# Optimization experiments

Measured on AMD Instinct MI355X. Metric: run time of the kernel, lower is better.

Reference implementation:

```python
import jax, jax.numpy as jnp
import numpy as np

T, B, S = 128, 128, 128
H, E, V, L = 1024, 512, 32000, 2


def setup_inputs() -> dict:
    key = jax.random.key(0)
    ks = jax.random.split(key, 16)
    s = 0.02
    inp = {
        "inputs": jax.random.randint(ks[0], (T, B), 0, V),
        "h0": jax.random.normal(ks[1], (L, B, H), jnp.float32) * 0.1,
        "c0": jax.random.normal(ks[2], (L, B, H), jnp.float32) * 0.1,
        "contexts": jax.random.normal(ks[3], (B, S, H), jnp.float32),
        "emb": jax.random.normal(ks[4], (V, E), jnp.float32) * s,
        "W_ih0": jax.random.normal(ks[5], (4 * H, E), jnp.float32) * s,
        "W_hh0": jax.random.normal(ks[6], (4 * H, H), jnp.float32) * s,
        "b_ih0": jnp.zeros((4 * H,), jnp.float32),
        "b_hh0": jnp.zeros((4 * H,), jnp.float32),
        "W_ih1": jax.random.normal(ks[7], (4 * H, H), jnp.float32) * s,
        "W_hh1": jax.random.normal(ks[8], (4 * H, H), jnp.float32) * s,
        "b_ih1": jnp.zeros((4 * H,), jnp.float32),
        "b_hh1": jnp.zeros((4 * H,), jnp.float32),
        "att_in_W": jax.random.normal(ks[9], (H, H), jnp.float32) * s,
        "att_in_b": jnp.zeros((H,), jnp.float32),
        "att_out_W": jax.random.normal(ks[10], (H, 2 * H), jnp.float32) * s,
        "att_out_b": jnp.zeros((H,), jnp.float32),
    }
    return inp


def _lstm_cell(x, h, c, Wih, Whh, bih, bhh):
    # torch.nn.LSTMCell: gates in (i, f, g, o) order
    gates = x @ Wih.T + bih + h @ Whh.T + bhh  # [B, 4H]
    i, f, g, o = jnp.split(gates, 4, axis=-1)
    c2 = jax.nn.sigmoid(f) * c + jax.nn.sigmoid(i) * jnp.tanh(g)
    h2 = jax.nn.sigmoid(o) * jnp.tanh(c2)
    return h2, c2


def reference(inputs, h0, c0, contexts, emb,
              W_ih0, W_hh0, b_ih0, b_hh0,
              W_ih1, W_hh1, b_ih1, b_hh1,
              att_in_W, att_in_b, att_out_W, att_out_b):
    layer_params = [(W_ih0, W_hh0, b_ih0, b_hh0), (W_ih1, W_hh1, b_ih1, b_hh1)]
    embs = emb[inputs]  # [T, B, E]

    def step(carry, x_t):
        h, c = carry  # each [L, B, H]
        x = x_t
        hs, cs = [], []
        for l, (Wih, Whh, bih, bhh) in enumerate(layer_params):
            h_l, c_l = _lstm_cell(x, h[l], c[l], Wih, Whh, bih, bhh)
            x = h_l  # dropout=0.0 / eval mode -> identity
            hs.append(h_l)
            cs.append(c_l)
        # global (Luong general) attention
        gamma = x @ att_in_W.T + att_in_b                     # [B, H]
        scores = jnp.einsum('bsh,bh->bs', contexts, gamma)    # [B, S]
        w = jax.nn.softmax(scores, axis=-1)
        c_t = jnp.einsum('bs,bsh->bh', w, contexts)           # [B, H]
        out = jnp.tanh(jnp.concatenate([c_t, x], axis=-1) @ att_out_W.T + att_out_b)
        return (jnp.stack(hs), jnp.stack(cs)), (out, w)

    (hT, cT), (outputs, attns) = jax.lax.scan(step, (h0, c0), embs)
    return outputs, hT, cT
```

## Files before the change

kernel.cpp:

```cpp
#include <hip/hip_runtime.h>

#define TT 128
#define BB 128
#define SS 128
#define HH 1024
#define EE 512
#define BH (BB*HH)

typedef unsigned short u16;
typedef __attribute__((ext_vector_type(8))) short s8v;
typedef __attribute__((ext_vector_type(4))) float f32x4;

__device__ __forceinline__ float b2f(u16 u) {
    union { unsigned int i; float f; } v; v.i = ((unsigned int)u) << 16; return v.f;
}
__device__ __forceinline__ u16 f2b(float f) {
    union { float f; unsigned int i; } v; v.f = f;
    unsigned int x = v.i;
    x = x + 0x7fffu + ((x >> 16) & 1u);
    return (u16)(x >> 16);
}
__device__ __forceinline__ float sigm(float x) {
    float t = __expf(-fabsf(x));
    float p = 1.0f / (1.0f + t);
    return x >= 0.0f ? p : 1.0f - p;
}
__device__ __forceinline__ float tanh_(float x) {
    float t = __expf(-2.0f * fabsf(x));
    float r = (1.0f - t) / (1.0f + t);
    return x >= 0.0f ? r : -r;
}

#define MFMA(a, b, c) __builtin_amdgcn_mfma_f32_16x16x32_bf16((a), (b), (c), 0, 0, 0)

__global__ __launch_bounds__(256)
void cvt_k(const float* __restrict__ s, u16* __restrict__ d, int n)
{
    const int i = (blockIdx.x * 256 + threadIdx.x) * 4;
    if (i < n) {
        const float4 v = *(const float4*)(s + i);
        ushort4 o;
        o.x = f2b(v.x); o.y = f2b(v.y); o.z = f2b(v.z); o.w = f2b(v.w);
        *(ushort4*)(d + i) = o;
    }
}

__global__ __launch_bounds__(128)
void gather_k(const int* __restrict__ toks, const float* __restrict__ emb,
              u16* __restrict__ X)
{
    const int row = blockIdx.x;
    const int tok = toks[row];
    const int c = threadIdx.x * 4;
    const float4 v = *(const float4*)(emb + (size_t)tok * EE + c);
    ushort4 o;
    o.x = f2b(v.x); o.y = f2b(v.y); o.z = f2b(v.z); o.w = f2b(v.w);
    *(ushort4*)(X + (size_t)row * EE + c) = o;
}

__global__ __launch_bounds__(256)
void init_k(const float* __restrict__ h0in,
            u16* __restrict__ h0ring, u16* __restrict__ h1init,
            int* __restrict__ barcnt)
{
    const int i = blockIdx.x * 256 + threadIdx.x;
    const u16 hb = f2b(h0in[i]);
    if (i < BH) h0ring[i] = hb;
    else        h1init[i - BH] = hb;
    if (i == 0) *barcnt = 0;
}

__global__ __launch_bounds__(512, 1)
void scan_k(const float* __restrict__ Wih0, const float* __restrict__ Whh0,
            const float* __restrict__ Wih1, const float* __restrict__ Whh1,
            const float* __restrict__ bih0, const float* __restrict__ bhh0,
            const float* __restrict__ bih1, const float* __restrict__ bhh1,
            const float* __restrict__ c0in,
            const u16* __restrict__ Xb,
            u16* __restrict__ h0ring,
            const u16* __restrict__ h1init,
            u16* __restrict__ H1all,
            float* __restrict__ outT,
            int* __restrict__ barcnt)
{
    extern __shared__ u16 lds[];
    u16* W0x = lds;
    u16* W0h = W0x + 16*4*16*8;
    u16* W1x = W0h + 32*4*16*8;
    u16* W1h = W1x + 32*4*16*8;
    float* gst = (float*)(W1h + 32*4*16*8);

    const int tid  = threadIdx.x;
    const int bk   = blockIdx.x;
    const int j0   = (((bk & 7) << 5) | (bk >> 3)) * 4;
    const int lane = tid & 63;
    const int w    = tid >> 6;
    const int l15  = lane & 15, quad = lane >> 4;

    auto loadW = [&](const float* src, int K, u16* dst) {
        const int ntup = (K / 32) * 4 * 16;
        for (int idx = tid; idx < ntup; idx += 512) {
            const int n = idx & 15, q = (idx >> 4) & 3, kc = idx >> 6;
            const int col = ((n >> 2) * HH) + j0 + (n & 3);
            const float* sp = src + (size_t)col * K + kc * 32 + q * 8;
            const float4 v0 = *(const float4*)(sp);
            const float4 v1 = *(const float4*)(sp + 4);
            u16* dp = dst + (size_t)idx * 8;
            dp[0] = f2b(v0.x); dp[1] = f2b(v0.y); dp[2] = f2b(v0.z); dp[3] = f2b(v0.w);
            dp[4] = f2b(v1.x); dp[5] = f2b(v1.y); dp[6] = f2b(v1.z); dp[7] = f2b(v1.w);
        }
    };
    loadW(Wih0, EE, W0x);
    loadW(Whh0, HH, W0h);
    loadW(Wih1, HH, W1x);
    loadW(Whh1, HH, W1h);

    const int prow = tid >> 2;
    const int pjj  = tid & 3;
    const int pj   = j0 + pjj;
    const int pw   = prow >> 4, pr16 = prow & 15;

    float c0 = c0in[(size_t)0 * BH + (size_t)prow * HH + pj];
    float c1 = c0in[(size_t)1 * BH + (size_t)prow * HH + pj];
    float b0[4], b1[4];
    #pragma unroll
    for (int g = 0; g < 4; ++g) {
        b0[g] = bih0[g * HH + pj] + bhh0[g * HH + pj];
        b1[g] = bih1[g * HH + pj] + bhh1[g * HH + pj];
    }

    __syncthreads();

    const int arow = w * 16 + l15;

    for (int p = 0; p <= TT; ++p) {
        f32x4 acc0 = (f32x4)0.0f, acc1 = (f32x4)0.0f;

        if (p < TT) {
            const u16* ap = Xb + ((size_t)p * BB + arow) * EE + quad * 8;
            #pragma unroll 8
            for (int kc = 0; kc < 16; ++kc) {
                s8v a = *(const s8v*)(ap + kc * 32);
                s8v b = *(const s8v*)(W0x + ((size_t)(kc * 4 + quad) * 16 + l15) * 8);
                acc0 = MFMA(a, b, acc0);
            }
        }

        if (p > 0) {
            if (tid == 0) {
                const int target = 256 * p;
                while (__hip_atomic_load(barcnt, __ATOMIC_RELAXED,
                                         __HIP_MEMORY_SCOPE_AGENT) < target) {
                    __builtin_amdgcn_s_sleep(2);
                }
            }
            __syncthreads();
            asm volatile("" ::: "memory");
        }

        const u16* h0p = h0ring + (size_t)p * BH;
        {
            const u16* ap = h0p + (size_t)arow * HH + quad * 8;
            if (p == 0) {
                #pragma unroll 8
                for (int kc = 0; kc < 32; ++kc) {
                    s8v a = *(const s8v*)(ap + kc * 32);
                    s8v b = *(const s8v*)(W0h + ((size_t)(kc * 4 + quad) * 16 + l15) * 8);
                    acc0 = MFMA(a, b, acc0);
                }
            } else if (p == TT) {
                #pragma unroll 8
                for (int kc = 0; kc < 32; ++kc) {
                    s8v a = *(const s8v*)(ap + kc * 32);
                    s8v b = *(const s8v*)(W1x + ((size_t)(kc * 4 + quad) * 16 + l15) * 8);
                    acc1 = MFMA(a, b, acc1);
                }
            } else {
                #pragma unroll 8
                for (int kc = 0; kc < 32; ++kc) {
                    s8v a = *(const s8v*)(ap + kc * 32);
                    s8v b0v = *(const s8v*)(W0h + ((size_t)(kc * 4 + quad) * 16 + l15) * 8);
                    s8v b1v = *(const s8v*)(W1x + ((size_t)(kc * 4 + quad) * 16 + l15) * 8);
                    acc0 = MFMA(a, b0v, acc0);
                    acc1 = MFMA(a, b1v, acc1);
                }
            }
        }
        if (p > 0) {
            const u16* h1p = (p == 1) ? h1init : (H1all + (size_t)(p - 2) * BH);
            const u16* ap = h1p + (size_t)arow * HH + quad * 8;
            #pragma unroll 8
            for (int kc = 0; kc < 32; ++kc) {
                s8v a = *(const s8v*)(ap + kc * 32);
                s8v b = *(const s8v*)(W1h + ((size_t)(kc * 4 + quad) * 16 + l15) * 8);
                acc1 = MFMA(a, b, acc1);
            }
        }

        if (p < TT) {
            #pragma unroll
            for (int r = 0; r < 4; ++r)
                gst[w * 320 + (quad * 4 + r) * 20 + l15] = acc0[r];
            __syncthreads();
            const float* gr = gst + pw * 320 + pr16 * 20;
            const float gi = gr[0 + pjj]  + b0[0];
            const float gf = gr[4 + pjj]  + b0[1];
            const float gg = gr[8 + pjj]  + b0[2];
            const float go = gr[12 + pjj] + b0[3];
            c0 = sigm(gf) * c0 + sigm(gi) * tanh_(gg);
            const float h = sigm(go) * tanh_(c0);
            h0ring[(size_t)(p + 1) * BH + (size_t)prow * HH + pj] = f2b(h);
            if (p == TT - 1) {
                outT[(size_t)0 * BH + (size_t)prow * HH + pj] = h;
                outT[(size_t)2 * BH + (size_t)prow * HH + pj] = c0;
            }
            __syncthreads();
        }
        if (p > 0) {
            #pragma unroll
            for (int r = 0; r < 4; ++r)
                gst[w * 320 + (quad * 4 + r) * 20 + l15] = acc1[r];
            __syncthreads();
            const float* gr = gst + pw * 320 + pr16 * 20;
            const float gi = gr[0 + pjj]  + b1[0];
            const float gf = gr[4 + pjj]  + b1[1];
            const float gg = gr[8 + pjj]  + b1[2];
            const float go = gr[12 + pjj] + b1[3];
            c1 = sigm(gf) * c1 + sigm(gi) * tanh_(gg);
            const float h = sigm(go) * tanh_(c1);
            H1all[(size_t)(p - 1) * BH + (size_t)prow * HH + pj] = f2b(h);
            if (p == TT) {
                outT[(size_t)1 * BH + (size_t)prow * HH + pj] = h;
                outT[(size_t)3 * BH + (size_t)prow * HH + pj] = c1;
            }
            __syncthreads();
        }

        if (p < TT && tid == 0) {
            __hip_atomic_fetch_add(barcnt, 1, __ATOMIC_RELEASE,
                                   __HIP_MEMORY_SCOPE_AGENT);
        }
    }
}

__global__ __launch_bounds__(256)
void gemm_bt_k(const u16* __restrict__ A1, int K1,
               const u16* __restrict__ A2, int K2,
               const u16* __restrict__ W, int ldw,
               const float* __restrict__ bias,
               u16* __restrict__ Cb, float* __restrict__ Cf,
               int N, int act)
{
    const int lane = threadIdx.x & 63;
    const int wave = threadIdx.x >> 6;
    const int l15 = lane & 15, quad = lane >> 4;
    const int n0 = blockIdx.x * 64;
    const int mrow = blockIdx.y * 64 + wave * 16;
    const int arow = mrow + l15;

    f32x4 acc[4];
    #pragma unroll
    for (int nt = 0; nt < 4; ++nt) acc[nt] = (f32x4)0.0f;

    const u16* wr0 = W + (size_t)(n0 + 0 * 16 + l15) * ldw + quad * 8;
    const u16* wr1 = W + (size_t)(n0 + 1 * 16 + l15) * ldw + quad * 8;
    const u16* wr2 = W + (size_t)(n0 + 2 * 16 + l15) * ldw + quad * 8;
    const u16* wr3 = W + (size_t)(n0 + 3 * 16 + l15) * ldw + quad * 8;

    {
        const u16* ap = A1 + (size_t)arow * K1 + quad * 8;
        #pragma unroll 4
        for (int kk = 0; kk < K1; kk += 32) {
            s8v a = *(const s8v*)(ap + kk);
            acc[0] = MFMA(a, *(const s8v*)(wr0 + kk), acc[0]);
            acc[1] = MFMA(a, *(const s8v*)(wr1 + kk), acc[1]);
            acc[2] = MFMA(a, *(const s8v*)(wr2 + kk), acc[2]);
            acc[3] = MFMA(a, *(const s8v*)(wr3 + kk), acc[3]);
        }
    }
    if (A2 != nullptr) {
        const u16* ap = A2 + (size_t)arow * K2 + quad * 8;
        #pragma unroll 4
        for (int kk = 0; kk < K2; kk += 32) {
            s8v a = *(const s8v*)(ap + kk);
            acc[0] = MFMA(a, *(const s8v*)(wr0 + K1 + kk), acc[0]);
            acc[1] = MFMA(a, *(const s8v*)(wr1 + K1 + kk), acc[1]);
            acc[2] = MFMA(a, *(const s8v*)(wr2 + K1 + kk), acc[2]);
            acc[3] = MFMA(a, *(const s8v*)(wr3 + K1 + kk), acc[3]);
        }
    }
    #pragma unroll
    for (int nt = 0; nt < 4; ++nt) {
        const int col = n0 + nt * 16 + l15;
        const float bv = bias[col];
        #pragma unroll
        for (int r = 0; r < 4; ++r) {
            const int row = mrow + quad * 4 + r;
            float v = acc[nt][r] + bv;
            if (act) v = tanh_(v);
            if (Cf) Cf[(size_t)row * N + col] = v;
            else    Cb[(size_t)row * N + col] = f2b(v);
        }
    }
}

__global__ __launch_bounds__(256)
void attn_k(const u16* __restrict__ gamma, const float* __restrict__ ctx,
            u16* __restrict__ ctall)
{
    const int b = blockIdx.x;
    const int t0 = blockIdx.y * 16;
    const int tid = threadIdx.x;
    const int lane = tid & 63, wave = tid >> 6;
    const int l15 = lane & 15, quad = lane >> 4;

    __shared__ float sw[16 * SS];

    {
        f32x4 acc0 = (f32x4)0.0f, acc1 = (f32x4)0.0f;
        const u16*   ap  = gamma + ((size_t)(t0 + l15) * BB + b) * HH + quad * 8;
        const float* bp0 = ctx + ((size_t)b * SS + (wave * 32 + l15)) * HH + quad * 8;
        const float* bp1 = ctx + ((size_t)b * SS + (wave * 32 + 16 + l15)) * HH + quad * 8;
        for (int kk = 0; kk < HH; kk += 32) {
            s8v a = *(const s8v*)(ap + kk);
            float4 u0 = *(const float4*)(bp0 + kk);
            float4 u1 = *(const float4*)(bp0 + kk + 4);
            s8v bv;
            bv[0] = (short)f2b(u0.x); bv[1] = (short)f2b(u0.y);
            bv[2] = (short)f2b(u0.z); bv[3] = (short)f2b(u0.w);
            bv[4] = (short)f2b(u1.x); bv[5] = (short)f2b(u1.y);
            bv[6] = (short)f2b(u1.z); bv[7] = (short)f2b(u1.w);
            acc0 = MFMA(a, bv, acc0);
            float4 w0 = *(const float4*)(bp1 + kk);
            float4 w1 = *(const float4*)(bp1 + kk + 4);
            s8v cv;
            cv[0] = (short)f2b(w0.x); cv[1] = (short)f2b(w0.y);
            cv[2] = (short)f2b(w0.z); cv[3] = (short)f2b(w0.w);
            cv[4] = (short)f2b(w1.x); cv[5] = (short)f2b(w1.y);
            cv[6] = (short)f2b(w1.z); cv[7] = (short)f2b(w1.w);
            acc1 = MFMA(a, cv, acc1);
        }
        #pragma unroll
        for (int r = 0; r < 4; ++r) {
            const int trow = quad * 4 + r;
            sw[trow * SS + wave * 32 + l15] = acc0[r];
            sw[trow * SS + wave * 32 + 16 + l15] = acc1[r];
        }
    }
    __syncthreads();

    {
        const int row = tid >> 4, c0 = tid & 15;
        float e[8];
        float m = -1e30f;
        #pragma unroll
        for (int k = 0; k < 8; ++k) { e[k] = sw[row * SS + c0 + k * 16]; m = fmaxf(m, e[k]); }
        #pragma unroll
        for (int off = 8; off >= 1; off >>= 1) m = fmaxf(m, __shfl_xor(m, off));
        float s = 0.0f;
        #pragma unroll
        for (int k = 0; k < 8; ++k) { e[k] = __expf(e[k] - m); s += e[k]; }
        #pragma unroll
        for (int off = 8; off >= 1; off >>= 1) s += __shfl_xor(s, off);
        const float inv = 1.0f / s;
        #pragma unroll
        for (int k = 0; k < 8; ++k) sw[row * SS + c0 + k * 16] = e[k] * inv;
    }
    __syncthreads();

    {
        const int h0 = tid * 4;
        float a[16][4];
        #pragma unroll
        for (int t = 0; t < 16; ++t)
            #pragma unroll
            for (int q = 0; q < 4; ++q) a[t][q] = 0.0f;

        const float* cp = ctx + (size_t)b * SS * HH + h0;
        for (int s = 0; s < SS; ++s) {
            const float4 cv = *(const float4*)(cp + (size_t)s * HH);
            #pragma unroll
            for (int t = 0; t < 16; ++t) {
                const float wgt = sw[t * SS + s];
                a[t][0] += wgt * cv.x;
                a[t][1] += wgt * cv.y;
                a[t][2] += wgt * cv.z;
                a[t][3] += wgt * cv.w;
            }
        }
        #pragma unroll
        for (int t = 0; t < 16; ++t) {
            u16* op = ctall + ((size_t)(t0 + t) * BB + b) * HH + h0;
            #pragma unroll
            for (int q = 0; q < 4; ++q) op[q] = f2b(a[t][q]);
        }
    }
}

extern "C" void kernel_launch(void* const* d_in, const int* in_sizes, int n_in,
                              void* d_out, int out_size, void* d_ws, size_t ws_size,
                              hipStream_t stream)
{
    const int*   toks = (const int*)d_in[0];
    const float* h0in = (const float*)d_in[1];
    const float* c0in = (const float*)d_in[2];
    const float* ctx  = (const float*)d_in[3];
    const float* emb  = (const float*)d_in[4];
    const float* Wih0 = (const float*)d_in[5];
    const float* Whh0 = (const float*)d_in[6];
    const float* bih0 = (const float*)d_in[7];
    const float* bhh0 = (const float*)d_in[8];
    const float* Wih1 = (const float*)d_in[9];
    const float* Whh1 = (const float*)d_in[10];
    const float* bih1 = (const float*)d_in[11];
    const float* bhh1 = (const float*)d_in[12];
    const float* attW = (const float*)d_in[13];
    const float* attb = (const float*)d_in[14];
    const float* outW = (const float*)d_in[15];
    const float* outb = (const float*)d_in[16];

    u16*   h0ring = (u16*)d_ws;
    u16*   h1init = h0ring + (size_t)(TT + 1) * BH;
    int*   barcnt = (int*)(h1init + BH);
    u16*   Xb     = (u16*)(barcnt + 64);
    u16*   H1all  = Xb + (size_t)TT * BB * EE;
    u16*   gammaA = H1all + (size_t)TT * BH;
    u16*   attWb  = gammaA + (size_t)TT * BH;
    u16*   outWb  = attWb + (size_t)HH * HH;
    u16*   ctall  = h0ring;

    cvt_k<<<dim3((HH * HH / 4 + 255) / 256), 256, 0, stream>>>(attW, attWb, HH * HH);
    cvt_k<<<dim3((2 * HH * HH / 4 + 255) / 256), 256, 0, stream>>>(outW, outWb, 2 * HH * HH);

    gather_k<<<dim3(TT * BB), 128, 0, stream>>>(toks, emb, Xb);
    init_k<<<dim3(2 * BH / 256), 256, 0, stream>>>(h0in, h0ring, h1init, barcnt);

    float* outp = (float*)d_out;
    const int ldsBytes = (16*4*16*8 + 3 * 32*4*16*8) * 2 + 8*16*20 * 4;
    hipFuncSetAttribute((const void*)scan_k,
                        hipFuncAttributeMaxDynamicSharedMemorySize, ldsBytes);
    scan_k<<<dim3(256), 512, ldsBytes, stream>>>(
        Wih0, Whh0, Wih1, Whh1, bih0, bhh0, bih1, bhh1, c0in,
        Xb, h0ring, h1init, H1all, outp + (size_t)TT * BH, barcnt);

    gemm_bt_k<<<dim3(HH / 64, (TT * BB) / 64), 256, 0, stream>>>(
        H1all, HH, nullptr, 0, attWb, HH, attb, gammaA, nullptr, HH, 0);

    attn_k<<<dim3(BB, TT / 16), 256, 0, stream>>>(gammaA, ctx, ctall);

    gemm_bt_k<<<dim3(HH / 64, (TT * BB) / 64), 256, 0, stream>>>(
        ctall, HH, H1all, HH, outWb, 2 * HH, outb, nullptr, outp, HH, 1);
}
```

Baseline: 4.297 ms.

## Split LSTM layers across two wave groups and use per-block flag barrier

The persistent scan kernel now runs 1024 threads per block. The first eight waves compute layer 0 gates and the second eight compute layer 1 gates concurrently, each with its own gate staging buffer, which removes the serialized two-phase update per step. The single atomic counter barrier is replaced with per-block progress flags: each block stores its step number and 256 threads poll one flag each. This adds register and occupancy pressure at 1024 threads and more polling traffic, in exchange for more MFMA parallelism per CU and less contention on the barrier.

```diff
diff --git a/kernel.cpp b/kernel.cpp
--- a/kernel.cpp
+++ b/kernel.cpp
@@ -61,16 +61,16 @@
 __global__ __launch_bounds__(256)
 void init_k(const float* __restrict__ h0in,
             u16* __restrict__ h0ring, u16* __restrict__ h1init,
-            int* __restrict__ barcnt)
+            int* __restrict__ flags)
 {
     const int i = blockIdx.x * 256 + threadIdx.x;
     const u16 hb = f2b(h0in[i]);
     if (i < BH) h0ring[i] = hb;
     else        h1init[i - BH] = hb;
-    if (i == 0) *barcnt = 0;
-}
-
-__global__ __launch_bounds__(512, 1)
+    if (i < 256) flags[i] = 0;
+}
+
+__global__ __launch_bounds__(1024, 1)
 void scan_k(const float* __restrict__ Wih0, const float* __restrict__ Whh0,
             const float* __restrict__ Wih1, const float* __restrict__ Whh1,
             const float* __restrict__ bih0, const float* __restrict__ bhh0,
@@ -81,25 +81,28 @@
             const u16* __restrict__ h1init,
             u16* __restrict__ H1all,
             float* __restrict__ outT,
-            int* __restrict__ barcnt)
+            int* __restrict__ flags)
 {
     extern __shared__ u16 lds[];
     u16* W0x = lds;
     u16* W0h = W0x + 16*4*16*8;
     u16* W1x = W0h + 32*4*16*8;
     u16* W1h = W1x + 32*4*16*8;
-    float* gst = (float*)(W1h + 32*4*16*8);
+    float* gst0 = (float*)(W1h + 32*4*16*8);
+    float* gst1 = gst0 + 8*16*20;
 
     const int tid  = threadIdx.x;
     const int bk   = blockIdx.x;
     const int j0   = (((bk & 7) << 5) | (bk >> 3)) * 4;
     const int lane = tid & 63;
     const int w    = tid >> 6;
+    const int wg   = w & 7;
+    const int grp  = w >> 3;
     const int l15  = lane & 15, quad = lane >> 4;
 
     auto loadW = [&](const float* src, int K, u16* dst) {
         const int ntup = (K / 32) * 4 * 16;
-        for (int idx = tid; idx < ntup; idx += 512) {
+        for (int idx = tid; idx < ntup; idx += 1024) {
             const int n = idx & 15, q = (idx >> 4) & 3, kc = idx >> 6;
             const int col = ((n >> 2) * HH) + j0 + (n & 3);
             const float* sp = src + (size_t)col * K + kc * 32 + q * 8;
@@ -115,43 +118,45 @@
     loadW(Wih1, HH, W1x);
     loadW(Whh1, HH, W1h);
 
-    const int prow = tid >> 2;
-    const int pjj  = tid & 3;
+    const int t2   = tid & 511;
+    const int prow = t2 >> 2;
+    const int pjj  = t2 & 3;
     const int pj   = j0 + pjj;
-    const int pw   = prow >> 4, pr16 = prow & 15;
-
-    float c0 = c0in[(size_t)0 * BH + (size_t)prow * HH + pj];
-    float c1 = c0in[(size_t)1 * BH + (size_t)prow * HH + pj];
-    float b0[4], b1[4];
-    #pragma unroll
-    for (int g = 0; g < 4; ++g) {
-        b0[g] = bih0[g * HH + pj] + bhh0[g * HH + pj];
-        b1[g] = bih1[g * HH + pj] + bhh1[g * HH + pj];
+    const int pw   = t2 >> 6;
+    const int pr16 = prow & 15;
+
+    const int lay = tid >> 9;
+    float cs = c0in[(size_t)lay * BH + (size_t)prow * HH + pj];
+    float bs[4];
+    {
+        const float* bihp = lay ? bih1 : bih0;
+        const float* bhhp = lay ? bhh1 : bhh0;
+        #pragma unroll
+        for (int g = 0; g < 4; ++g) bs[g] = bihp[g * HH + pj] + bhhp[g * HH + pj];
     }
 
     __syncthreads();
 
-    const int arow = w * 16 + l15;
+    const int arow = wg * 16 + l15;
 
     for (int p = 0; p <= TT; ++p) {
-        f32x4 acc0 = (f32x4)0.0f, acc1 = (f32x4)0.0f;
-
-        if (p < TT) {
+        f32x4 acc = (f32x4)0.0f;
+
+        if (grp == 0 && p < TT) {
             const u16* ap = Xb + ((size_t)p * BB + arow) * EE + quad * 8;
             #pragma unroll 8
             for (int kc = 0; kc < 16; ++kc) {
                 s8v a = *(const s8v*)(ap + kc * 32);
                 s8v b = *(const s8v*)(W0x + ((size_t)(kc * 4 + quad) * 16 + l15) * 8);
-                acc0 = MFMA(a, b, acc0);
+                acc = MFMA(a, b, acc);
             }
         }
 
         if (p > 0) {
-            if (tid == 0) {
-                const int target = 256 * p;
-                while (__hip_atomic_load(barcnt, __ATOMIC_RELAXED,
-                                         __HIP_MEMORY_SCOPE_AGENT) < target) {
-                    __builtin_amdgcn_s_sleep(2);
+            if (tid >= 512 && tid < 768) {
+                while (__hip_atomic_load(&flags[tid - 512], __ATOMIC_RELAXED,
+                                         __HIP_MEMORY_SCOPE_AGENT) < p) {
+                    __builtin_amdgcn_s_sleep(1);
                 }
             }
             __syncthreads();
@@ -159,86 +164,68 @@
         }
 
         const u16* h0p = h0ring + (size_t)p * BH;
-        {
-            const u16* ap = h0p + (size_t)arow * HH + quad * 8;
-            if (p == 0) {
+        if (grp == 0) {
+            if (p < TT) {
+                const u16* ap = h0p + (size_t)arow * HH + quad * 8;
                 #pragma unroll 8
                 for (int kc = 0; kc < 32; ++kc) {
                     s8v a = *(const s8v*)(ap + kc * 32);
                     s8v b = *(const s8v*)(W0h + ((size_t)(kc * 4 + quad) * 16 + l15) * 8);
-                    acc0 = MFMA(a, b, acc0);
+                    acc = MFMA(a, b, acc);
                 }
-            } else if (p == TT) {
-                #pragma unroll 8
-                for (int kc = 0; kc < 32; ++kc) {
-                    s8v a = *(const s8v*)(ap + kc * 32);
-                    s8v b = *(const s8v*)(W1x + ((size_t)(kc * 4 + quad) * 16 + l15) * 8);
-                    acc1 = MFMA(a, b, acc1);
+            }
+        } else if (p > 0) {
+            const u16* ap0 = h0p + (size_t)arow * HH + quad * 8;
+            const u16* h1p = (p == 1) ? h1init : (H1all + (size_t)(p - 2) * BH);
+            const u16* ap1 = h1p + (size_t)arow * HH + quad * 8;
+            #pragma unroll 8
+            for (int kc = 0; kc < 32; ++kc) {
+                s8v a0 = *(const s8v*)(ap0 + kc * 32);
+                s8v b0 = *(const s8v*)(W1x + ((size_t)(kc * 4 + quad) * 16 + l15) * 8);
+                acc = MFMA(a0, b0, acc);
+                s8v a1 = *(const s8v*)(ap1 + kc * 32);
+                s8v b1 = *(const s8v*)(W1h + ((size_t)(kc * 4 + quad) * 16 + l15) * 8);
+                acc = MFMA(a1, b1, acc);
+            }
+        }
+
+        {
+            float* gw = (grp == 0) ? gst0 : gst1;
+            #pragma unroll
+            for (int r = 0; r < 4; ++r)
+                gw[wg * 320 + (quad * 4 + r) * 20 + l15] = acc[r];
+        }
+        const bool active = lay ? (p > 0) : (p < TT);
+        if (active) {
+            const float* gr = (lay ? gst1 : gst0) + pw * 320 + pr16 * 20;
+            const float gi = gr[0 + pjj]  + bs[0];
+            const float gf = gr[4 + pjj]  + bs[1];
+            const float gg = gr[8 + pjj]  + bs[2];
+            const float go = gr[12 + pjj] + bs[3];
+            cs = sigm(gf) * cs + sigm(gi) * tanh_(gg);
+            const float h = sigm(go) * tanh_(cs);
+            const u16 hb = f2b(h);
+            if (lay == 0) {
+                h0ring[(size_t)(p + 1) * BH + (size_t)prow * HH + pj] = hb;
+                if (p == TT - 1) {
+                    outT[(size_t)0 * BH + (size_t)prow * HH + pj] = h;
+                    outT[(size_t)2 * BH + (size_t)prow * HH + pj] = cs;
                 }
             } else {
-                #pragma unroll 8
-                for (int kc = 0; kc < 32; ++kc) {
-                    s8v a = *(const s8v*)(ap + kc * 32);
-                    s8v b0v = *(const s8v*)(W0h + ((size_t)(kc * 4 + quad) * 16 + l15) * 8);
-                    s8v b1v = *(const s8v*)(W1x + ((size_t)(kc * 4 + quad) * 16 + l15) * 8);
-                    acc0 = MFMA(a, b0v, acc0);
-                    acc1 = MFMA(a, b1v, acc1);
+                H1all[(size_t)(p - 1) * BH + (size_t)prow * HH + pj] = hb;
+                if (p == TT) {
+                    outT[(size_t)1 * BH + (size_t)prow * HH + pj] = h;
+                    outT[(size_t)3 * BH + (size_t)prow * HH + pj] = cs;
                 }
             }
         }
-        if (p > 0) {
-            const u16* h1p = (p == 1) ? h1init : (H1all + (size_t)(p - 2) * BH);
-            const u16* ap = h1p + (size_t)arow * HH + quad * 8;
-            #pragma unroll 8
-            for (int kc = 0; kc < 32; ++kc) {
-                s8v a = *(const s8v*)(ap + kc * 32);
-                s8v b = *(const s8v*)(W1h + ((size_t)(kc * 4 + quad) * 16 + l15) * 8);
-                acc1 = MFMA(a, b, acc1);
-            }
-        }
 
         if (p < TT) {
-            #pragma unroll
-            for (int r = 0; r < 4; ++r)
-                gst[w * 320 + (quad * 4 + r) * 20 + l15] = acc0[r];
             __syncthreads();
-            const float* gr = gst + pw * 320 + pr16 * 20;
-            const float gi = gr[0 + pjj]  + b0[0];
-            const float gf = gr[4 + pjj]  + b0[1];
-            const float gg = gr[8 + pjj]  + b0[2];
-            const float go = gr[12 + pjj] + b0[3];
-            c0 = sigm(gf) * c0 + sigm(gi) * tanh_(gg);
-            const float h = sigm(go) * tanh_(c0);
-            h0ring[(size_t)(p + 1) * BH + (size_t)prow * HH + pj] = f2b(h);
-            if (p == TT - 1) {
-                outT[(size_t)0 * BH + (size_t)prow * HH + pj] = h;
-                outT[(size_t)2 * BH + (size_t)prow * HH + pj] = c0;
-            }
-            __syncthreads();
-        }
-        if (p > 0) {
-            #pragma unroll
-            for (int r = 0; r < 4; ++r)
-                gst[w * 320 + (quad * 4 + r) * 20 + l15] = acc1[r];
-            __syncthreads();
-            const float* gr = gst + pw * 320 + pr16 * 20;
-            const float gi = gr[0 + pjj]  + b1[0];
-            const float gf = gr[4 + pjj]  + b1[1];
-            const float gg = gr[8 + pjj]  + b1[2];
-            const float go = gr[12 + pjj] + b1[3];
-            c1 = sigm(gf) * c1 + sigm(gi) * tanh_(gg);
-            const float h = sigm(go) * tanh_(c1);
-            H1all[(size_t)(p - 1) * BH + (size_t)prow * HH + pj] = f2b(h);
-            if (p == TT) {
-                outT[(size_t)1 * BH + (size_t)prow * HH + pj] = h;
-                outT[(size_t)3 * BH + (size_t)prow * HH + pj] = c1;
-            }
-            __syncthreads();
-        }
-
-        if (p < TT && tid == 0) {
-            __hip_atomic_fetch_add(barcnt, 1, __ATOMIC_RELEASE,
+            if (tid == 0) {
+                __hip_atomic_store(&flags[bk], p + 1, __ATOMIC_RELEASE,
                                    __HIP_MEMORY_SCOPE_AGENT);
+            }
         }
     }
 }
@@ -421,8 +408,8 @@
 
     u16*   h0ring = (u16*)d_ws;
     u16*   h1init = h0ring + (size_t)(TT + 1) * BH;
-    int*   barcnt = (int*)(h1init + BH);
-    u16*   Xb     = (u16*)(barcnt + 64);
+    int*   flags  = (int*)(h1init + BH);
+    u16*   Xb     = (u16*)(flags + 256);
     u16*   H1all  = Xb + (size_t)TT * BB * EE;
     u16*   gammaA = H1all + (size_t)TT * BH;
     u16*   attWb  = gammaA + (size_t)TT * BH;
@@ -433,15 +420,15 @@
     cvt_k<<<dim3((2 * HH * HH / 4 + 255) / 256), 256, 0, stream>>>(outW, outWb, 2 * HH * HH);
 
     gather_k<<<dim3(TT * BB), 128, 0, stream>>>(toks, emb, Xb);
-    init_k<<<dim3(2 * BH / 256), 256, 0, stream>>>(h0in, h0ring, h1init, barcnt);
+    init_k<<<dim3(2 * BH / 256), 256, 0, stream>>>(h0in, h0ring, h1init, flags);
 
     float* outp = (float*)d_out;
-    const int ldsBytes = (16*4*16*8 + 3 * 32*4*16*8) * 2 + 8*16*20 * 4;
+    const int ldsBytes = (16*4*16*8 + 3 * 32*4*16*8) * 2 + 2 * 8*16*20 * 4;
     hipFuncSetAttribute((const void*)scan_k,
                         hipFuncAttributeMaxDynamicSharedMemorySize, ldsBytes);
-    scan_k<<<dim3(256), 512, ldsBytes, stream>>>(
+    scan_k<<<dim3(256), 1024, ldsBytes, stream>>>(
         Wih0, Whh0, Wih1, Whh1, bih0, bhh0, bih1, bhh1, c0in,
-        Xb, h0ring, h1init, H1all, outp + (size_t)TT * BH, barcnt);
+        Xb, h0ring, h1init, H1all, outp + (size_t)TT * BH, flags);
 
     gemm_bt_k<<<dim3(HH / 64, (TT * BB) / 64), 256, 0, stream>>>(
         H1all, HH, nullptr, 0, attWb, HH, attb, gammaA, nullptr, HH, 0);
```

Measured after the change: 4.916 ms. +14.4%, slower.
